# Performance work log

Hardware: AMD Instinct MI355X
Metric: run time of the kernel (lower is better)

## Reference

```python
import jax, jax.numpy as jnp
import numpy as np

B, S, D = 16, 2048, 1024
NEG_BIG = 1e9  # additive mask constant from original code


def setup_inputs() -> dict:
    key0 = jax.random.key(0)
    kq, kk, kv, km = jax.random.split(key0, 4)
    query = jax.random.normal(kq, (B, S, D), dtype=jnp.float32)
    key = jax.random.normal(kk, (B, S, D), dtype=jnp.float32)
    value = jax.random.normal(kv, (B, S, D), dtype=jnp.float32)
    mask = jax.random.randint(km, (B, S), 0, 2).astype(jnp.bool_)
    return {"query": query, "key": key, "value": value, "mask": mask}


def reference(query, key, value, mask):
    # e[b,i,j] = <query[b,i], key[b,j]> / sqrt(D)
    d = query.shape[-1]
    scale = 1.0 / jnp.sqrt(jnp.asarray(d, dtype=query.dtype))
    e = jnp.einsum('bid,bjd->bij', query, key) * scale
    # Original: e -= (1 - expand_dims(mask, -1)) * 1e9  -> masks along row (query) axis
    m = mask.astype(query.dtype)[:, :, None]  # [B, S, 1]
    e = e - (1.0 - m) * NEG_BIG
    a = jax.nn.softmax(e, axis=-1)            # [B, S, S]
    return jnp.einsum('bij,bjd->bid', a, value)
```

## Files before the change

kernel.cpp:

```cpp
#include <hip/hip_runtime.h>
#include <math.h>

#define B_ 16
#define S_ 2048
#define D_ 1024
#define SCALE 0.03125f

typedef __bf16 bf16;
typedef __bf16 bf16x8 __attribute__((ext_vector_type(8)));
typedef float f32x4 __attribute__((ext_vector_type(4)));

#define MFMA(a, b, c) __builtin_amdgcn_mfma_f32_16x16x32_bf16((a), (b), (c), 0, 0, 0)

#define BAR()                                           \
  do {                                                  \
    asm volatile("s_waitcnt lgkmcnt(0)" ::: "memory");  \
    __builtin_amdgcn_s_barrier();                       \
    asm volatile("" ::: "memory");                      \
  } while (0)

__global__ __launch_bounds__(256) void prep_kernel(const float* __restrict__ K,
                                                   const float* __restrict__ V,
                                                   bf16* __restrict__ Kr,
                                                   bf16* __restrict__ Vr) {
  __shared__ bf16 tile[64][136];
  const int jt = blockIdx.x;
  const int w = blockIdx.y;
  const int b = blockIdx.z & 15;
  const int isV = blockIdx.z >> 4;
  const int t = threadIdx.x;
  const float* src = (isV ? V : K) + ((size_t)b * S_ + jt * 64) * D_ + w * 128;
#pragma unroll
  for (int p = 0; p < 8; ++p) {
    const int f4 = p * 256 + t;
    const int row = f4 >> 5;
    const int c4 = (f4 & 31) * 4;
    float4 v = *(const float4*)(src + (size_t)row * D_ + c4);
    tile[row][c4 + 0] = (bf16)v.x;
    tile[row][c4 + 1] = (bf16)v.y;
    tile[row][c4 + 2] = (bf16)v.z;
    tile[row][c4 + 3] = (bf16)v.w;
  }
  __syncthreads();
  bf16* dst = (isV ? Vr : Kr) + (((size_t)b * 32 + jt) * 8 + w) * 8192;
  if (!isV) {
#pragma unroll
    for (int p = 0; p < 4; ++p) {
      const int g = p * 256 + t;
      const int l = g & 63;
      const int nt = (g >> 6) & 3;
      const int kc = g >> 8;
      bf16x8 o =
          *(const bf16x8*)&tile[nt * 16 + (l & 15)][kc * 32 + (l >> 4) * 8];
      *(bf16x8*)(dst + (size_t)g * 8) = o;
    }
  } else {
#pragma unroll
    for (int p = 0; p < 4; ++p) {
      const int g = p * 256 + t;
      const int l = g & 63;
      const int nt = (g >> 6) & 7;
      const int ks = g >> 9;
      const int sr = ks * 32 + (l >> 4) * 8;
      const int dc = nt * 16 + (l & 15);
      bf16x8 o;
#pragma unroll
      for (int j = 0; j < 8; ++j) o[j] = tile[sr + j][dc];
      *(bf16x8*)(dst + (size_t)g * 8) = o;
    }
  }
}

__global__ __launch_bounds__(512, 2) void attn_kernel(
    const float* __restrict__ Q, const bf16* __restrict__ Kr,
    const bf16* __restrict__ Vr, const int* __restrict__ mask,
    float* __restrict__ out) {
  __shared__ float sc[8][32][68];
  __shared__ bf16 pbuf[32][72];
  __shared__ float madd[32];
  __shared__ float mS[32], lS[32], alphaS[32];

  const int d = blockIdx.x;
  const int b = ((d & 7) << 1) | ((d >> 3) & 1);
  const int q0 = (d >> 4) * 32;
  const int t = threadIdx.x;
  const int w = t >> 6;
  const int lane = t & 63;
  const int n16 = lane & 15;
  const int q4 = lane >> 4;
  const int ds0 = w * 128;

  if (t < 32) {
    madd[t] = mask[b * S_ + q0 + t] ? 0.0f : 1e9f;
    mS[t] = -1e30f;
    lS[t] = 0.0f;
  }

  const float* Qb = Q + (size_t)b * S_ * D_;
  const bf16* Kw = Kr + ((size_t)b * 256 + w) * 8192 + (size_t)lane * 8;
  const bf16* Vw = Vr + ((size_t)b * 256 + w) * 8192 + (size_t)lane * 8;

  bf16x8 qf[2][4];
#pragma unroll
  for (int mt = 0; mt < 2; ++mt)
#pragma unroll
    for (int kc = 0; kc < 4; ++kc) {
      const float* qp = Qb + (size_t)(q0 + 16 * mt + n16) * D_ +
                        ds0 + kc * 32 + q4 * 8;
      float4 a = *(const float4*)qp;
      float4 c = *(const float4*)(qp + 4);
      bf16x8 f;
      f[0] = (bf16)a.x; f[1] = (bf16)a.y; f[2] = (bf16)a.z; f[3] = (bf16)a.w;
      f[4] = (bf16)c.x; f[5] = (bf16)c.y; f[6] = (bf16)c.z; f[7] = (bf16)c.w;
      qf[mt][kc] = f;
    }

  f32x4 o[2][8];
#pragma unroll
  for (int mt = 0; mt < 2; ++mt)
#pragma unroll
    for (int nt = 0; nt < 8; ++nt) o[mt][nt] = (f32x4){0.f, 0.f, 0.f, 0.f};

  __syncthreads();

  for (int jt = 0; jt < 32; ++jt) {
    const bf16* kb = Kw + (size_t)jt * 65536;
    const bf16* vb = Vw + (size_t)jt * 65536;

    bf16x8 kf[4][4];
#pragma unroll
    for (int kc = 0; kc < 4; ++kc)
#pragma unroll
      for (int nt = 0; nt < 4; ++nt)
        kf[nt][kc] = *(const bf16x8*)(kb + ((kc * 4 + nt) << 9));
    f32x4 acc[2][4];
#pragma unroll
    for (int mt = 0; mt < 2; ++mt)
#pragma unroll
      for (int nt = 0; nt < 4; ++nt) acc[mt][nt] = (f32x4){0.f, 0.f, 0.f, 0.f};
#pragma unroll
    for (int kc = 0; kc < 4; ++kc)
#pragma unroll
      for (int nt = 0; nt < 4; ++nt)
#pragma unroll
        for (int mt = 0; mt < 2; ++mt)
          acc[mt][nt] = MFMA(qf[mt][kc], kf[nt][kc], acc[mt][nt]);

    bf16x8 vf[2][8];
#pragma unroll
    for (int ks = 0; ks < 2; ++ks)
#pragma unroll
      for (int nt = 0; nt < 8; ++nt)
        vf[ks][nt] = *(const bf16x8*)(vb + ((ks * 8 + nt) << 9));

#pragma unroll
    for (int mt = 0; mt < 2; ++mt)
#pragma unroll
      for (int nt = 0; nt < 4; ++nt)
#pragma unroll
        for (int r = 0; r < 4; ++r)
          sc[w][16 * mt + 4 * q4 + r][nt * 16 + n16] = acc[mt][nt][r];
    BAR();

    {
      const int r = t >> 4;
      const int cg = t & 15;
      const int c0 = cg * 4;
      float s0v = 0.f, s1v = 0.f, s2v = 0.f, s3v = 0.f;
#pragma unroll
      for (int ww = 0; ww < 8; ++ww) {
        float4 v = *(const float4*)&sc[ww][r][c0];
        s0v += v.x; s1v += v.y; s2v += v.z; s3v += v.w;
      }
      const float ma = madd[r];
      s0v = s0v * SCALE - ma;
      s1v = s1v * SCALE - ma;
      s2v = s2v * SCALE - ma;
      s3v = s3v * SCALE - ma;
      float mx = fmaxf(fmaxf(s0v, s1v), fmaxf(s2v, s3v));
      mx = fmaxf(mx, __shfl_xor(mx, 1));
      mx = fmaxf(mx, __shfl_xor(mx, 2));
      mx = fmaxf(mx, __shfl_xor(mx, 4));
      mx = fmaxf(mx, __shfl_xor(mx, 8));
      const float m_old = mS[r];
      const float m_new = fmaxf(m_old, mx);
      const float p0 = __expf(s0v - m_new);
      const float p1 = __expf(s1v - m_new);
      const float p2 = __expf(s2v - m_new);
      const float p3 = __expf(s3v - m_new);
      float ps = (p0 + p1) + (p2 + p3);
      ps += __shfl_xor(ps, 1);
      ps += __shfl_xor(ps, 2);
      ps += __shfl_xor(ps, 4);
      ps += __shfl_xor(ps, 8);
      if (cg == 0) {
        const float al = __expf(m_old - m_new);
        alphaS[r] = al;
        lS[r] = lS[r] * al + ps;
        mS[r] = m_new;
      }
      pbuf[r][c0 + 0] = (bf16)p0;
      pbuf[r][c0 + 1] = (bf16)p1;
      pbuf[r][c0 + 2] = (bf16)p2;
      pbuf[r][c0 + 3] = (bf16)p3;
    }
    BAR();

    f32x4 av[2];
#pragma unroll
    for (int mt = 0; mt < 2; ++mt)
#pragma unroll
      for (int rg = 0; rg < 4; ++rg) av[mt][rg] = alphaS[16 * mt + 4 * q4 + rg];
#pragma unroll
    for (int mt = 0; mt < 2; ++mt)
#pragma unroll
      for (int nt = 0; nt < 8; ++nt) o[mt][nt] *= av[mt];

    bf16x8 pf[2][2];
#pragma unroll
    for (int mt = 0; mt < 2; ++mt)
#pragma unroll
      for (int ks = 0; ks < 2; ++ks)
        pf[mt][ks] = *(const bf16x8*)&pbuf[16 * mt + n16][ks * 32 + q4 * 8];

#pragma unroll
    for (int ks = 0; ks < 2; ++ks)
#pragma unroll
      for (int nt = 0; nt < 8; ++nt)
#pragma unroll
        for (int mt = 0; mt < 2; ++mt)
          o[mt][nt] = MFMA(pf[mt][ks], vf[ks][nt], o[mt][nt]);
  }

  f32x4 invl[2];
#pragma unroll
  for (int mt = 0; mt < 2; ++mt)
#pragma unroll
    for (int rg = 0; rg < 4; ++rg)
      invl[mt][rg] = 1.0f / lS[16 * mt + 4 * q4 + rg];
#pragma unroll
  for (int mt = 0; mt < 2; ++mt)
#pragma unroll
    for (int nt = 0; nt < 8; ++nt)
#pragma unroll
      for (int rg = 0; rg < 4; ++rg) {
        const size_t row = (size_t)b * S_ + q0 + 16 * mt + 4 * q4 + rg;
        out[row * D_ + ds0 + nt * 16 + n16] = o[mt][nt][rg] * invl[mt][rg];
      }
}

extern "C" void kernel_launch(void* const* d_in, const int* in_sizes, int n_in,
                              void* d_out, int out_size, void* d_ws, size_t ws_size,
                              hipStream_t stream) {
  (void)in_sizes; (void)n_in; (void)out_size; (void)ws_size;
  const float* Q = (const float*)d_in[0];
  const float* K = (const float*)d_in[1];
  const float* V = (const float*)d_in[2];
  const int* mask = (const int*)d_in[3];
  float* out = (float*)d_out;
  bf16* Kr = (bf16*)d_ws;
  bf16* Vr = (bf16*)d_ws + (size_t)B_ * S_ * D_;

  prep_kernel<<<dim3(32, 8, 32), 256, 0, stream>>>(K, V, Kr, Vr);
  attn_kernel<<<B_ * (S_ / 32), 512, 0, stream>>>(Q, Kr, Vr, mask, out);
}
```

Baseline: 859.6 us.

## Prefetch next K tile, restructure softmax reduction, drop LDS staging in prep

```diff
diff --git a/kernel.cpp b/kernel.cpp
--- a/kernel.cpp
+++ b/kernel.cpp
@@ -7,6 +7,7 @@
 #define SCALE 0.03125f
 
 typedef __bf16 bf16;
+typedef __bf16 bf16x4v __attribute__((ext_vector_type(4)));
 typedef __bf16 bf16x8 __attribute__((ext_vector_type(8)));
 typedef float f32x4 __attribute__((ext_vector_type(4)));
 
@@ -23,51 +24,36 @@
                                                    const float* __restrict__ V,
                                                    bf16* __restrict__ Kr,
                                                    bf16* __restrict__ Vr) {
-  __shared__ bf16 tile[64][136];
-  const int jt = blockIdx.x;
-  const int w = blockIdx.y;
-  const int b = blockIdx.z & 15;
-  const int isV = blockIdx.z >> 4;
+  const int jt = blockIdx.x, w = blockIdx.y, b = blockIdx.z;
   const int t = threadIdx.x;
-  const float* src = (isV ? V : K) + ((size_t)b * S_ + jt * 64) * D_ + w * 128;
-#pragma unroll
-  for (int p = 0; p < 8; ++p) {
-    const int f4 = p * 256 + t;
-    const int row = f4 >> 5;
-    const int c4 = (f4 & 31) * 4;
-    float4 v = *(const float4*)(src + (size_t)row * D_ + c4);
-    tile[row][c4 + 0] = (bf16)v.x;
-    tile[row][c4 + 1] = (bf16)v.y;
-    tile[row][c4 + 2] = (bf16)v.z;
-    tile[row][c4 + 3] = (bf16)v.w;
+  const size_t sbase = ((size_t)b * S_ + jt * 64) * D_ + w * 128;
+  bf16* kd = Kr + (((size_t)b * 32 + jt) * 8 + w) * 8192;
+  bf16* vd = Vr + (((size_t)b * 32 + jt) * 8 + w) * 8192;
+#pragma unroll
+  for (int p = 0; p < 4; ++p) {
+    const int g = p * 256 + t;
+    const int l = g & 63, f = g >> 6;
+    const int kc = f >> 2, nt = f & 3;
+    const float* sp = K + sbase + (size_t)(nt * 16 + (l & 15)) * D_ +
+                      kc * 32 + (l >> 4) * 8;
+    float4 a = *(const float4*)sp;
+    float4 c = *(const float4*)(sp + 4);
+    bf16x8 o;
+    o[0] = (bf16)a.x; o[1] = (bf16)a.y; o[2] = (bf16)a.z; o[3] = (bf16)a.w;
+    o[4] = (bf16)c.x; o[5] = (bf16)c.y; o[6] = (bf16)c.z; o[7] = (bf16)c.w;
+    *(bf16x8*)(kd + (size_t)g * 8) = o;
   }
-  __syncthreads();
-  bf16* dst = (isV ? Vr : Kr) + (((size_t)b * 32 + jt) * 8 + w) * 8192;
-  if (!isV) {
-#pragma unroll
-    for (int p = 0; p < 4; ++p) {
-      const int g = p * 256 + t;
-      const int l = g & 63;
-      const int nt = (g >> 6) & 3;
-      const int kc = g >> 8;
-      bf16x8 o =
-          *(const bf16x8*)&tile[nt * 16 + (l & 15)][kc * 32 + (l >> 4) * 8];
-      *(bf16x8*)(dst + (size_t)g * 8) = o;
-    }
-  } else {
-#pragma unroll
-    for (int p = 0; p < 4; ++p) {
-      const int g = p * 256 + t;
-      const int l = g & 63;
-      const int nt = (g >> 6) & 7;
-      const int ks = g >> 9;
-      const int sr = ks * 32 + (l >> 4) * 8;
-      const int dc = nt * 16 + (l & 15);
-      bf16x8 o;
-#pragma unroll
-      for (int j = 0; j < 8; ++j) o[j] = tile[sr + j][dc];
-      *(bf16x8*)(dst + (size_t)g * 8) = o;
-    }
+#pragma unroll
+  for (int p = 0; p < 4; ++p) {
+    const int g = p * 256 + t;
+    const int l = g & 63, f = g >> 6;
+    const int ks = f >> 3, nt = f & 7;
+    const float* sp = V + sbase + (size_t)(ks * 32 + (l >> 4) * 8) * D_ +
+                      nt * 16 + (l & 15);
+    bf16x8 o;
+#pragma unroll
+    for (int j = 0; j < 8; ++j) o[j] = (bf16)sp[(size_t)j * D_];
+    *(bf16x8*)(vd + (size_t)g * 8) = o;
   }
 }
 
@@ -75,10 +61,9 @@
     const float* __restrict__ Q, const bf16* __restrict__ Kr,
     const bf16* __restrict__ Vr, const int* __restrict__ mask,
     float* __restrict__ out) {
-  __shared__ float sc[8][32][68];
+  __shared__ f32x4 scv[8][8][64];
   __shared__ bf16 pbuf[32][72];
-  __shared__ float madd[32];
-  __shared__ float mS[32], lS[32], alphaS[32];
+  __shared__ float alphaS[32], lS[32];
 
   const int d = blockIdx.x;
   const int b = ((d & 7) << 1) | ((d >> 3) & 1);
@@ -90,15 +75,13 @@
   const int q4 = lane >> 4;
   const int ds0 = w * 128;
 
-  if (t < 32) {
-    madd[t] = mask[b * S_ + q0 + t] ? 0.0f : 1e9f;
-    mS[t] = -1e30f;
-    lS[t] = 0.0f;
-  }
-
   const float* Qb = Q + (size_t)b * S_ * D_;
   const bf16* Kw = Kr + ((size_t)b * 256 + w) * 8192 + (size_t)lane * 8;
   const bf16* Vw = Vr + ((size_t)b * 256 + w) * 8192 + (size_t)lane * 8;
+
+  const int prow = 4 * w + (lane & 3);
+  const float ma = mask[b * S_ + q0 + prow] ? 0.0f : 1e9f;
+  float m_run = -1e30f, l_run = 0.0f;
 
   bf16x8 qf[2][4];
 #pragma unroll
@@ -121,31 +104,35 @@
 #pragma unroll
     for (int nt = 0; nt < 8; ++nt) o[mt][nt] = (f32x4){0.f, 0.f, 0.f, 0.f};
 
-  __syncthreads();
-
-  for (int jt = 0; jt < 32; ++jt) {
-    const bf16* kb = Kw + (size_t)jt * 65536;
+  bf16x8 kfA[4][4], kfB[4][4];
+#pragma unroll
+  for (int kc = 0; kc < 4; ++kc)
+#pragma unroll
+    for (int nt = 0; nt < 4; ++nt)
+      kfA[nt][kc] = *(const bf16x8*)(Kw + ((kc * 4 + nt) << 9));
+
+  auto body = [&](int jt, bf16x8 (&kfC)[4][4], bf16x8 (&kfN)[4][4]) {
+    f32x4 acc[2][4];
+#pragma unroll
+    for (int mt = 0; mt < 2; ++mt)
+#pragma unroll
+      for (int nt = 0; nt < 4; ++nt) acc[mt][nt] = (f32x4){0.f, 0.f, 0.f, 0.f};
+    __builtin_amdgcn_s_setprio(1);
+#pragma unroll
+    for (int kc = 0; kc < 4; ++kc)
+#pragma unroll
+      for (int nt = 0; nt < 4; ++nt)
+#pragma unroll
+        for (int mt = 0; mt < 2; ++mt)
+          acc[mt][nt] = MFMA(qf[mt][kc], kfC[nt][kc], acc[mt][nt]);
+    __builtin_amdgcn_s_setprio(0);
+
+#pragma unroll
+    for (int mt = 0; mt < 2; ++mt)
+#pragma unroll
+      for (int nt = 0; nt < 4; ++nt) scv[w][mt * 4 + nt][lane] = acc[mt][nt];
+
     const bf16* vb = Vw + (size_t)jt * 65536;
-
-    bf16x8 kf[4][4];
-#pragma unroll
-    for (int kc = 0; kc < 4; ++kc)
-#pragma unroll
-      for (int nt = 0; nt < 4; ++nt)
-        kf[nt][kc] = *(const bf16x8*)(kb + ((kc * 4 + nt) << 9));
-    f32x4 acc[2][4];
-#pragma unroll
-    for (int mt = 0; mt < 2; ++mt)
-#pragma unroll
-      for (int nt = 0; nt < 4; ++nt) acc[mt][nt] = (f32x4){0.f, 0.f, 0.f, 0.f};
-#pragma unroll
-    for (int kc = 0; kc < 4; ++kc)
-#pragma unroll
-      for (int nt = 0; nt < 4; ++nt)
-#pragma unroll
-        for (int mt = 0; mt < 2; ++mt)
-          acc[mt][nt] = MFMA(qf[mt][kc], kf[nt][kc], acc[mt][nt]);
-
     bf16x8 vf[2][8];
 #pragma unroll
     for (int ks = 0; ks < 2; ++ks)
@@ -153,56 +140,55 @@
       for (int nt = 0; nt < 8; ++nt)
         vf[ks][nt] = *(const bf16x8*)(vb + ((ks * 8 + nt) << 9));
 
-#pragma unroll
-    for (int mt = 0; mt < 2; ++mt)
+    const bf16* kbn = Kw + (size_t)((jt + 1) & 31) * 65536;
+#pragma unroll
+    for (int kc = 0; kc < 4; ++kc)
 #pragma unroll
       for (int nt = 0; nt < 4; ++nt)
-#pragma unroll
-        for (int r = 0; r < 4; ++r)
-          sc[w][16 * mt + 4 * q4 + r][nt * 16 + n16] = acc[mt][nt][r];
+        kfN[nt][kc] = *(const bf16x8*)(kbn + ((kc * 4 + nt) << 9));
     BAR();
 
     {
-      const int r = t >> 4;
-      const int cg = t & 15;
-      const int c0 = cg * 4;
-      float s0v = 0.f, s1v = 0.f, s2v = 0.f, s3v = 0.f;
-#pragma unroll
-      for (int ww = 0; ww < 8; ++ww) {
-        float4 v = *(const float4*)&sc[ww][r][c0];
-        s0v += v.x; s1v += v.y; s2v += v.z; s3v += v.w;
-      }
-      const float ma = madd[r];
-      s0v = s0v * SCALE - ma;
-      s1v = s1v * SCALE - ma;
-      s2v = s2v * SCALE - ma;
-      s3v = s3v * SCALE - ma;
-      float mx = fmaxf(fmaxf(s0v, s1v), fmaxf(s2v, s3v));
-      mx = fmaxf(mx, __shfl_xor(mx, 1));
-      mx = fmaxf(mx, __shfl_xor(mx, 2));
+      const int fsel = (w >> 2) * 4 + (lane >> 4);
+      const int lidx = (w & 3) * 16 + n16;
+      f32x4 s = scv[0][fsel][lidx];
+#pragma unroll
+      for (int ww = 1; ww < 8; ++ww) s += scv[ww][fsel][lidx];
+      float t0, t1;
+      t0 = (lane & 1) ? s[0] : s[1]; t0 = __shfl_xor(t0, 1);
+      t1 = (lane & 1) ? s[2] : s[3]; t1 = __shfl_xor(t1, 1);
+      s[0] = (lane & 1) ? t0 : s[0]; s[1] = (lane & 1) ? s[1] : t0;
+      s[2] = (lane & 1) ? t1 : s[2]; s[3] = (lane & 1) ? s[3] : t1;
+      t0 = (lane & 2) ? s[0] : s[2]; t0 = __shfl_xor(t0, 2);
+      t1 = (lane & 2) ? s[1] : s[3]; t1 = __shfl_xor(t1, 2);
+      s[0] = (lane & 2) ? t0 : s[0]; s[2] = (lane & 2) ? s[2] : t0;
+      s[1] = (lane & 2) ? t1 : s[1]; s[3] = (lane & 2) ? s[3] : t1;
+      s[0] = s[0] * SCALE - ma;
+      s[1] = s[1] * SCALE - ma;
+      s[2] = s[2] * SCALE - ma;
+      s[3] = s[3] * SCALE - ma;
+      float mx = fmaxf(fmaxf(s[0], s[1]), fmaxf(s[2], s[3]));
       mx = fmaxf(mx, __shfl_xor(mx, 4));
       mx = fmaxf(mx, __shfl_xor(mx, 8));
-      const float m_old = mS[r];
-      const float m_new = fmaxf(m_old, mx);
-      const float p0 = __expf(s0v - m_new);
-      const float p1 = __expf(s1v - m_new);
-      const float p2 = __expf(s2v - m_new);
-      const float p3 = __expf(s3v - m_new);
+      mx = fmaxf(mx, __shfl_xor(mx, 16));
+      mx = fmaxf(mx, __shfl_xor(mx, 32));
+      const float m_new = fmaxf(m_run, mx);
+      const float alpha = __expf(m_run - m_new);
+      const float p0 = __expf(s[0] - m_new);
+      const float p1 = __expf(s[1] - m_new);
+      const float p2 = __expf(s[2] - m_new);
+      const float p3 = __expf(s[3] - m_new);
       float ps = (p0 + p1) + (p2 + p3);
-      ps += __shfl_xor(ps, 1);
-      ps += __shfl_xor(ps, 2);
       ps += __shfl_xor(ps, 4);
       ps += __shfl_xor(ps, 8);
-      if (cg == 0) {
-        const float al = __expf(m_old - m_new);
-        alphaS[r] = al;
-        lS[r] = lS[r] * al + ps;
-        mS[r] = m_new;
-      }
-      pbuf[r][c0 + 0] = (bf16)p0;
-      pbuf[r][c0 + 1] = (bf16)p1;
-      pbuf[r][c0 + 2] = (bf16)p2;
-      pbuf[r][c0 + 3] = (bf16)p3;
+      ps += __shfl_xor(ps, 16);
+      ps += __shfl_xor(ps, 32);
+      l_run = l_run * alpha + ps;
+      m_run = m_new;
+      if (lane < 4) alphaS[4 * w + lane] = alpha;
+      bf16x4v pk;
+      pk[0] = (bf16)p0; pk[1] = (bf16)p1; pk[2] = (bf16)p2; pk[3] = (bf16)p3;
+      *(bf16x4v*)&pbuf[prow][(lane >> 2) * 4] = pk;
     }
     BAR();
 
@@ -223,6 +209,7 @@
       for (int ks = 0; ks < 2; ++ks)
         pf[mt][ks] = *(const bf16x8*)&pbuf[16 * mt + n16][ks * 32 + q4 * 8];
 
+    __builtin_amdgcn_s_setprio(1);
 #pragma unroll
     for (int ks = 0; ks < 2; ++ks)
 #pragma unroll
@@ -230,8 +217,16 @@
 #pragma unroll
         for (int mt = 0; mt < 2; ++mt)
           o[mt][nt] = MFMA(pf[mt][ks], vf[ks][nt], o[mt][nt]);
+    __builtin_amdgcn_s_setprio(0);
+  };
+
+  for (int jt = 0; jt < 32; jt += 2) {
+    body(jt, kfA, kfB);
+    body(jt + 1, kfB, kfA);
   }
 
+  if (lane < 4) lS[4 * w + lane] = l_run;
+  BAR();
   f32x4 invl[2];
 #pragma unroll
   for (int mt = 0; mt < 2; ++mt)
@@ -261,6 +256,6 @@
   bf16* Kr = (bf16*)d_ws;
   bf16* Vr = (bf16*)d_ws + (size_t)B_ * S_ * D_;
 
-  prep_kernel<<<dim3(32, 8, 32), 256, 0, stream>>>(K, V, Kr, Vr);
+  prep_kernel<<<dim3(32, 8, B_), 256, 0, stream>>>(K, V, Kr, Vr);
   attn_kernel<<<B_ * (S_ / 32), 512, 0, stream>>>(Q, Kr, Vr, mask, out);
 }
```

After: 1.103 ms. +28.3%, slower.
